# Performance work log

Hardware: AMD Instinct MI355X
Metric: run time of the kernel (lower is better)

Reference implementation:

```python
import jax, jax.numpy as jnp
import numpy as np

BN_EPS = 1e-6
SOFTMAX_EPS = 1e-8
D = 64      # fingerprint_dim
BD = 12     # bond_dim
N_ATOM = 10000
N_EDGE = 40000


def _bn(x, gamma, beta, mean, var):
    # BatchNorm1d in inference mode (running stats)
    return (x - mean) / jnp.sqrt(var + BN_EPS) * gamma + beta


def setup_inputs() -> dict:
    key = jax.random.key(0)
    ks = jax.random.split(key, 16)
    inp = {
        "atom": jax.random.normal(ks[0], (N_ATOM, D), dtype=jnp.float32),
        "bond_index": jax.random.randint(ks[1], (N_EDGE, 2), 0, N_ATOM, dtype=jnp.int64),
        "bond": jax.random.normal(ks[2], (N_EDGE, BD), dtype=jnp.float32),
        # encoder: Linear(bond_dim, D*D) + BatchNorm1d(D*D)
        "enc_W": jax.random.normal(ks[3], (D * D, BD), dtype=jnp.float32) * (1.0 / np.sqrt(BD)),
        "enc_b": jnp.zeros((D * D,), dtype=jnp.float32),
        "enc_gamma": jnp.ones((D * D,), dtype=jnp.float32),
        "enc_beta": jnp.zeros((D * D,), dtype=jnp.float32),
        "enc_mean": jnp.zeros((D * D,), dtype=jnp.float32),
        "enc_var": jnp.ones((D * D,), dtype=jnp.float32),
        # align: Linear(2*D, 1)
        "align_W": jax.random.normal(ks[4], (1, 2 * D), dtype=jnp.float32) * (1.0 / np.sqrt(2 * D)),
        "align_b": jnp.zeros((1,), dtype=jnp.float32),
        # attend: Linear(D, D) + BatchNorm1d(D), no activation
        "att_W": jax.random.normal(ks[5], (D, D), dtype=jnp.float32) * (1.0 / np.sqrt(D)),
        "att_b": jnp.zeros((D,), dtype=jnp.float32),
        "att_gamma": jnp.ones((D,), dtype=jnp.float32),
        "att_beta": jnp.zeros((D,), dtype=jnp.float32),
        "att_mean": jnp.zeros((D,), dtype=jnp.float32),
        "att_var": jnp.ones((D,), dtype=jnp.float32),
        # GRUCell(D, D)
        "gru_W_ih": jax.random.normal(ks[6], (3 * D, D), dtype=jnp.float32) * (1.0 / np.sqrt(D)),
        "gru_W_hh": jax.random.normal(ks[7], (3 * D, D), dtype=jnp.float32) * (1.0 / np.sqrt(D)),
        "gru_b_ih": jnp.zeros((3 * D,), dtype=jnp.float32),
        "gru_b_hh": jnp.zeros((3 * D,), dtype=jnp.float32),
    }
    return inp


def reference(atom, bond_index, bond,
              enc_W, enc_b, enc_gamma, enc_beta, enc_mean, enc_var,
              align_W, align_b,
              att_W, att_b, att_gamma, att_beta, att_mean, att_var,
              gru_W_ih, gru_W_hh, gru_b_ih, gru_b_hh):
    num_atom, d = atom.shape
    tgt = bond_index[:, 0]  # target atom of each edge
    nbr = bond_index[:, 1]  # neighbor atom of each edge

    # encoder: relu(BN(linear(bond))) -> per-edge [d, d] bond matrix
    enc = jax.nn.relu(_bn(bond @ enc_W.T + enc_b, enc_gamma, enc_beta, enc_mean, enc_var))
    enc = enc.reshape(-1, d, d)  # [E, d, d]

    # gather neighbor atoms, per-edge matvec through bond matrix
    neighbor = jnp.einsum('ed,edf->ef', atom[nbr], enc)  # [E, d]

    # attention logits (dropout is identity in eval)
    feat = jnp.concatenate([atom[tgt], neighbor], axis=-1)  # [E, 2d]
    score = jax.nn.leaky_relu(feat @ align_W.T + align_b, negative_slope=0.01)  # [E, 1]

    # segment softmax over target atoms
    mx = jax.ops.segment_max(score, tgt, num_segments=num_atom)  # [N, 1]
    ex = jnp.exp(score - mx[tgt])
    denom = jax.ops.segment_sum(ex, tgt, num_segments=num_atom)[tgt] + SOFTMAX_EPS
    attn = ex / denom  # [E, 1]

    # attend: BN(linear(neighbor)) (no activation), weighted scatter-add
    attd = _bn(neighbor @ att_W.T + att_b, att_gamma, att_beta, att_mean, att_var)
    context = jax.ops.segment_sum(attn * attd, tgt, num_segments=num_atom)  # [N, d]
    context = jax.nn.elu(context)

    # GRUCell(context, atom)
    gi = context @ gru_W_ih.T + gru_b_ih  # [N, 3d]
    gh = atom @ gru_W_hh.T + gru_b_hh     # [N, 3d]
    i_r, i_z, i_n = jnp.split(gi, 3, axis=-1)
    h_r, h_z, h_n = jnp.split(gh, 3, axis=-1)
    r = jax.nn.sigmoid(i_r + h_r)
    z = jax.nn.sigmoid(i_z + h_z)
    n = jnp.tanh(i_n + r * h_n)
    return (1.0 - z) * n + z * atom
```

## Files before the change

kernel.cpp:

```cpp
#include <hip/hip_runtime.h>
#include <math.h>

#define NA 10000
#define NE 40000

typedef float f4 __attribute__((ext_vector_type(4)));
typedef float f16v __attribute__((ext_vector_type(16)));
typedef int   i4 __attribute__((ext_vector_type(4)));
typedef __bf16 bf16x8 __attribute__((ext_vector_type(8)));

union U8 { unsigned short us[8]; bf16x8 v; };

static __device__ __forceinline__ unsigned short bf_rne(float x){
  unsigned u = __float_as_uint(x);
  unsigned r = (u + 0x7fffu + ((u>>16)&1u)) >> 16;
  return (unsigned short)r;
}
static __device__ __forceinline__ float bf_to_f(unsigned short h){
  return __uint_as_float(((unsigned)h)<<16);
}

__global__ __launch_bounds__(256) void k_pre(
  const float* __restrict__ encW, const float* __restrict__ encB,
  const float* __restrict__ eg, const float* __restrict__ ebt,
  const float* __restrict__ e_mn, const float* __restrict__ e_vr,
  const float* __restrict__ attW, const float* __restrict__ attB,
  const float* __restrict__ agm, const float* __restrict__ abt,
  const float* __restrict__ amn, const float* __restrict__ avr,
  const float* __restrict__ wih, const float* __restrict__ whh,
  const int* __restrict__ bidx, const float* __restrict__ atom,
  const float* __restrict__ alW,
  unsigned short* __restrict__ Bh, unsigned short* __restrict__ Bl,
  unsigned short* __restrict__ aBh, unsigned short* __restrict__ aBl,
  float* __restrict__ attBf, float* __restrict__ wT,
  float* __restrict__ p, int* __restrict__ cnt)
{
  int tid = threadIdx.x;
  int gid = blockIdx.x*256 + tid;
  int gstride = gridDim.x*256;
  for (int i=gid; i<65536; i+=gstride){
    int j = i&7, ll = (i>>3)&63, t = i>>9;
    int d = t>>1, ft = t&1;
    int k = ((ll>>5)<<3)+j;
    int n = d*64 + ft*32 + (ll&31);
    float s = eg[n]*rsqrtf(e_vr[n]+1e-6f);
    unsigned short vh=0, vl=0;
    if (k<12){
      float wv = encW[n*12+k]*s;
      unsigned short hi = bf_rne(wv);
      vh = hi; vl = bf_rne(wv - bf_to_f(hi));
    } else if (k==12){
      float b = (encB[n]-e_mn[n])*s + ebt[n];
      unsigned short hi = bf_rne(b);
      vh = hi; vl = bf_rne(b - bf_to_f(hi));
    }
    Bh[i] = vh; Bl[i] = vl;
  }
  for (int i=gid; i<4096; i+=gstride){
    int j=i&7, l=(i>>3)&63, t=i>>9;
    int kk=t>>1, nt=t&1;
    int k = kk*16 + ((l>>5)<<3) + j;
    int n = nt*32 + (l&31);
    float s = agm[n]*rsqrtf(avr[n]+1e-6f);
    float wv = attW[n*64+k]*s;
    unsigned short hi = bf_rne(wv);
    aBh[i]=hi; aBl[i]=bf_rne(wv - bf_to_f(hi));
  }
  for (int f=gid; f<64; f+=gstride){
    float s = agm[f]*rsqrtf(avr[f]+1e-6f);
    attBf[f] = (attB[f]-amn[f])*s + abt[f];
  }
  for (int i=gid; i<24576; i+=gstride){
    int j=i&3, f=(i>>2)&63, idx2=i>>8;
    int g=idx2>>4, kg=idx2&15, k=kg*4+j;
    wT[i] = (g<3)? wih[(g*64+f)*64+k] : whh[((g-3)*64+f)*64+k];
  }
  {
    int wid = gid>>6;
    int l = tid&63;
    float wl = alW[l];
    for (int a=wid; a<NA; a+=(gstride>>6)){
      float v = wl*atom[(size_t)a*64+l];
      v += __shfl_xor(v,1);  v += __shfl_xor(v,2);
      v += __shfl_xor(v,4);  v += __shfl_xor(v,8);
      v += __shfl_xor(v,16); v += __shfl_xor(v,32);
      if (l==0) p[a]=v;
    }
  }
  for (int e=gid; e<NE; e+=gstride) atomicAdd(&cnt[bidx[e*2]],1);
}

__global__ __launch_bounds__(256) void k_scan(const int* __restrict__ cnt,
                                              int* __restrict__ rowstart,
                                              int* __restrict__ wofs)
{
  __shared__ int sPart[256];
  int t = threadIdx.x;
  int base = t*40;
  i4 buf[10];
  int sum = 0;
  if (base < NA){
    const i4* cp = (const i4*)(cnt + base);
    #pragma unroll
    for (int i=0;i<10;i++) buf[i] = cp[i];
    #pragma unroll
    for (int i=0;i<10;i++) sum += buf[i].x+buf[i].y+buf[i].z+buf[i].w;
  }
  sPart[t]=sum;
  __syncthreads();
  for (int off=1; off<256; off<<=1){
    int v = (t>=off)? sPart[t-off] : 0;
    __syncthreads();
    sPart[t]+=v;
    __syncthreads();
  }
  int run = sPart[t]-sum;
  if (base < NA){
    #pragma unroll
    for (int i=0;i<10;i++){
      i4 b=buf[i], o;
      o.x=run; run+=b.x; o.y=run; run+=b.y;
      o.z=run; run+=b.z; o.w=run; run+=b.w;
      ((i4*)(rowstart+base))[i]=o;
      ((i4*)(wofs+base))[i]=o;
    }
  }
  if (t==0) rowstart[NA]=NE;
}

__global__ __launch_bounds__(256) void k_scatter(const int* __restrict__ bidx,
                                                 int* __restrict__ wofs,
                                                 int* __restrict__ elist)
{
  int e = blockIdx.x*256 + threadIdx.x;
  if (e < NE){
    int tg = bidx[e*2];
    int pos = atomicAdd(&wofs[tg],1);
    elist[pos]=e;
  }
}

__global__ __launch_bounds__(256) void k_edge(
  const float* __restrict__ atom, const int* __restrict__ bidx, const float* __restrict__ bond,
  const unsigned short* __restrict__ Bh, const unsigned short* __restrict__ Bl,
  const int* __restrict__ elist, float* __restrict__ nbC)
{
  __shared__ float sA[2304];
  __shared__ float sP[4096];
  __shared__ int   sEl[32];
  __shared__ int   sNbr[32];

  int tid = threadIdx.x;
  int l = tid & 63;
  int w = tid >> 6;
  int g = l >> 5;
  int em = l & 31;
  int E0 = blockIdx.x * 32;

  if (tid < 32){
    int e = elist[E0+tid];
    sEl[tid] = e;
    sNbr[tid] = bidx[e*2+1];
  }
  __syncthreads();
  for (int i=tid; i<2048; i+=256){
    int le=i>>6, d=i&63;
    sA[d*36+le] = atom[(size_t)sNbr[le]*64 + d];
  }

  U8 A1, A2;
  {
    const f4* bp = (const f4*)(bond + (size_t)sEl[em]*12);
    f4 b0=bp[0], b1v=bp[1], b2v=bp[2];
    float bv[12] = {b0.x,b0.y,b0.z,b0.w,b1v.x,b1v.y,b1v.z,b1v.w,b2v.x,b2v.y,b2v.z,b2v.w};
    unsigned short hi[12], lo2[12];
    #pragma unroll
    for (int j=0;j<12;j++){ hi[j]=bf_rne(bv[j]); lo2[j]=bf_rne(bv[j]-bf_to_f(hi[j])); }
    #pragma unroll
    for (int j=0;j<8;j++){
      int k = g*8+j;
      A1.us[j] = (k<12)? hi[k] : (k==12? (unsigned short)0x3F80 : (unsigned short)0);
      A2.us[j] = (k<12)? lo2[k] : (unsigned short)0;
    }
  }
  __syncthreads();

  int ft = w & 1;
  int dbase = (w >> 1) * 32;

  f4 nacc[4];
  #pragma unroll
  for (int q=0;q<4;q++) nacc[q] = (f4){0.f,0.f,0.f,0.f};
  f16v cz;
  #pragma unroll
  for (int r=0;r<16;r++) cz[r] = 0.f;

  U8 cbh, cbl;
  cbh.v = *(const bf16x8*)(Bh + ((size_t)((dbase*2+ft)*64 + l))*8);
  cbl.v = *(const bf16x8*)(Bl + ((size_t)((dbase*2+ft)*64 + l))*8);

  #pragma unroll 2
  for (int dd=0; dd<32; dd++){
    int d = dbase + dd;
    int dn = (dd<31)? d+1 : d;
    U8 nbh, nbl;
    nbh.v = *(const bf16x8*)(Bh + ((size_t)((dn*2+ft)*64 + l))*8);
    nbl.v = *(const bf16x8*)(Bl + ((size_t)((dn*2+ft)*64 + l))*8);

    f4 ldA[4];
    #pragma unroll
    for (int q=0;q<4;q++) ldA[q] = *(const f4*)&sA[d*36 + 8*q + 4*g];

    f16v c;
    c = __builtin_amdgcn_mfma_f32_32x32x16_bf16(A1.v, cbh.v, cz, 0,0,0);
    c = __builtin_amdgcn_mfma_f32_32x32x16_bf16(A2.v, cbh.v, c, 0,0,0);
    c = __builtin_amdgcn_mfma_f32_32x32x16_bf16(A1.v, cbl.v, c, 0,0,0);
    #pragma unroll
    for (int r=0;r<16;r++){
      float ev = fmaxf(c[r], 0.f);
      nacc[r>>2][r&3] = fmaf(ldA[r>>2][r&3], ev, nacc[r>>2][r&3]);
    }
    cbh = nbh; cbl = nbl;
  }

  #pragma unroll
  for (int r=0;r<16;r++)
    sP[w*1024 + r*64 + l] = nacc[r>>2][r&3];
  __syncthreads();

  if (w < 2){
    #pragma unroll 4
    for (int r=0;r<16;r++){
      int idx = r*64 + l;
      float v = sP[w*1024 + idx] + sP[(w+2)*1024 + idx];
      int m = (r&3) + ((r>>2)<<3) + ((l>>5)<<2);
      int f = (w<<5) + (l&31);
      nbC[(size_t)(E0+m)*64 + f] = v;
    }
  }
}

__global__ __launch_bounds__(256) void k_zq(
  const float* __restrict__ nbC,
  const unsigned short* __restrict__ aBh, const unsigned short* __restrict__ aBl,
  const float* __restrict__ alW,
  float* __restrict__ zC, float* __restrict__ qv)
{
  __shared__ float sNb[64*68];
  int tid = threadIdx.x;
  int l = tid & 63;
  int w = tid >> 6;
  int g = l >> 5;
  int em = l & 31;
  int E0 = blockIdx.x * 64;

  for (int i=tid; i<4096; i+=256){
    int le=i>>6, f=i&63;
    sNb[le*68+f] = nbC[(size_t)(E0+le)*64 + f];
  }
  __syncthreads();

  {
    float alwn = alW[64+l];
    #pragma unroll 4
    for (int i=0;i<16;i++){
      int le = w*16 + i;
      float qq = sNb[le*68 + l] * alwn;
      qq += __shfl_xor(qq,1);  qq += __shfl_xor(qq,2);
      qq += __shfl_xor(qq,4);  qq += __shfl_xor(qq,8);
      qq += __shfl_xor(qq,16); qq += __shfl_xor(qq,32);
      if (l==0) qv[E0+le] = qq;
    }
  }

  {
    f16v c;
    #pragma unroll
    for (int r=0;r<16;r++) c[r] = 0.f;
    int mt2 = w>>1, nt = w&1;
    #pragma unroll
    for (int kk=0; kk<4; kk++){
      const float* src = &sNb[(mt2*32+em)*68 + kk*16 + g*8];
      f4 x0 = *(const f4*)src;
      f4 x1 = *(const f4*)(src+4);
      U8 Ah, Al;
      #pragma unroll
      for (int j=0;j<4;j++){
        unsigned short h0 = bf_rne(x0[j]);
        Ah.us[j] = h0; Al.us[j] = bf_rne(x0[j]-bf_to_f(h0));
        unsigned short h1 = bf_rne(x1[j]);
        Ah.us[4+j] = h1; Al.us[4+j] = bf_rne(x1[j]-bf_to_f(h1));
      }
      U8 bh, bl;
      bh.v = *(const bf16x8*)(aBh + ((size_t)((kk*2+nt)*64 + l))*8);
      bl.v = *(const bf16x8*)(aBl + ((size_t)((kk*2+nt)*64 + l))*8);
      c = __builtin_amdgcn_mfma_f32_32x32x16_bf16(Ah.v, bh.v, c, 0,0,0);
      c = __builtin_amdgcn_mfma_f32_32x32x16_bf16(Al.v, bh.v, c, 0,0,0);
      c = __builtin_amdgcn_mfma_f32_32x32x16_bf16(Ah.v, bl.v, c, 0,0,0);
    }
    #pragma unroll
    for (int r=0;r<16;r++){
      int row = (r&3) + ((r>>2)<<3) + ((l>>5)<<2);
      zC[(size_t)(E0 + mt2*32 + row)*64 + nt*32 + (l&31)] = c[r];
    }
  }
}

__global__ __launch_bounds__(256, 4) void k_gru(
  const float* __restrict__ atom, const float* __restrict__ zC,
  const int* __restrict__ rowstart, const float* __restrict__ p,
  const float* __restrict__ qv, const float* __restrict__ alB,
  const float* __restrict__ attBf, const float* __restrict__ wT,
  const float* __restrict__ bih, const float* __restrict__ bhh,
  float* __restrict__ out)
{
  __shared__ float sc[4][2][64];
  __shared__ float shh[4][2][64];
  int tid = threadIdx.x;
  int l = tid & 63;
  int w = tid >> 6;
  int base = blockIdx.x*8 + w*2;
  float bias = attBf[l];
  float ab = alB[0];

  #pragma unroll
  for (int aa=0; aa<2; aa++){
    int a = base + aa;
    float cf=0.f, hf=0.f;
    if (a < NA){
      hf = atom[(size_t)a*64 + l];
      int d0 = rowstart[a];
      int deg = rowstart[a+1] - d0;
      if (deg > 0){
        float pa = p[a] + ab;
        float mx = -1e30f;
        #pragma unroll 1
        for (int i=0;i<deg;i++){
          float s = pa + qv[d0+i];
          s = (s>0.f)? s : 0.01f*s;
          mx = fmaxf(mx, s);
        }
        float dn = 0.f, y = 0.f;
        #pragma unroll 1
        for (int i=0;i<deg;i++){
          float s = pa + qv[d0+i];
          s = (s>0.f)? s : 0.01f*s;
          float ex = __expf(s - mx);
          dn += ex;
          y = fmaf(ex, zC[(size_t)(d0+i)*64 + l], y);
        }
        cf = (y + dn*bias)/(dn + 1e-8f);
        cf = (cf>0.f)? cf : expm1f(cf);
      }
    }
    sc[w][aa][l] = cf; shh[w][aa][l] = hf;
  }
  __syncthreads();

  float acc[6][2];
  #pragma unroll
  for (int gg=0;gg<6;gg++){ acc[gg][0]=0.f; acc[gg][1]=0.f; }

  #pragma unroll 2
  for (int kg=0; kg<16; kg++){
    f4 wv[6];
    #pragma unroll
    for (int gg=0;gg<6;gg++) wv[gg] = *(const f4*)&wT[(size_t)((gg*16+kg)*64 + l)*4];
    #pragma unroll
    for (int aa=0;aa<2;aa++){
      f4 cv = *(const f4*)&sc[w][aa][kg*4];
      f4 hv = *(const f4*)&shh[w][aa][kg*4];
      #pragma unroll
      for (int j=0;j<4;j++){
        acc[0][aa] = fmaf(cv[j], wv[0][j], acc[0][aa]);
        acc[1][aa] = fmaf(cv[j], wv[1][j], acc[1][aa]);
        acc[2][aa] = fmaf(cv[j], wv[2][j], acc[2][aa]);
        acc[3][aa] = fmaf(hv[j], wv[3][j], acc[3][aa]);
        acc[4][aa] = fmaf(hv[j], wv[4][j], acc[4][aa]);
        acc[5][aa] = fmaf(hv[j], wv[5][j], acc[5][aa]);
      }
    }
  }

  float b0 = bih[l], b1 = bih[64+l], b2 = bih[128+l];
  float h0 = bhh[l], h1 = bhh[64+l], h2 = bhh[128+l];
  #pragma unroll
  for (int aa=0;aa<2;aa++){
    int a = base + aa;
    if (a < NA){
      float hf = shh[w][aa][l];
      float r = 1.f/(1.f + expf(-(acc[0][aa] + b0 + acc[3][aa] + h0)));
      float z = 1.f/(1.f + expf(-(acc[1][aa] + b1 + acc[4][aa] + h1)));
      float n = tanhf(acc[2][aa] + b2 + r*(acc[5][aa] + h2));
      out[(size_t)a*64 + l] = (1.f - z)*n + z*hf;
    }
  }
}

extern "C" void kernel_launch(void* const* d_in, const int* in_sizes, int n_in,
                              void* d_out, int out_size, void* d_ws, size_t ws_size,
                              hipStream_t stream) {
  const float* atom = (const float*)d_in[0];
  const int*   bidx = (const int*)  d_in[1];
  const float* bond = (const float*)d_in[2];
  const float* encW = (const float*)d_in[3];
  const float* encB = (const float*)d_in[4];
  const float* eg   = (const float*)d_in[5];
  const float* ebt  = (const float*)d_in[6];
  const float* e_mn = (const float*)d_in[7];
  const float* e_vr = (const float*)d_in[8];
  const float* alW  = (const float*)d_in[9];
  const float* alB  = (const float*)d_in[10];
  const float* atW  = (const float*)d_in[11];
  const float* atB  = (const float*)d_in[12];
  const float* agm  = (const float*)d_in[13];
  const float* abt  = (const float*)d_in[14];
  const float* amn  = (const float*)d_in[15];
  const float* avr  = (const float*)d_in[16];
  const float* wih  = (const float*)d_in[17];
  const float* whh  = (const float*)d_in[18];
  const float* bih  = (const float*)d_in[19];
  const float* bhh  = (const float*)d_in[20];

  float* ws = (float*)d_ws;
  unsigned short* Bh  = (unsigned short*)(ws + 0);
  unsigned short* Bl  = (unsigned short*)(ws + 32768);
  unsigned short* aBh = (unsigned short*)(ws + 65536);
  unsigned short* aBl = (unsigned short*)(ws + 67584);
  float* attBf   = ws + 69632;
  float* wT      = ws + 69696;
  float* p       = ws + 94272;
  int*   cnt     = (int*)(ws + 104288);
  int*   rowstart= (int*)(ws + 114304);
  int*   wofs    = (int*)(ws + 124320);
  int*   elist   = (int*)(ws + 134336);
  float* qv      = ws + 174336;
  float* nbC     = ws + 214336;
  float* outp    = (float*)d_out;

  hipMemsetAsync(cnt, 0, NA*sizeof(int), stream);
  k_pre<<<512, 256, 0, stream>>>(encW,encB,eg,ebt,e_mn,e_vr,
                                 atW,atB,agm,abt,amn,avr,
                                 wih,whh,bidx,atom,alW,
                                 Bh,Bl,aBh,aBl,attBf,wT,p,cnt);
  k_scan<<<1, 256, 0, stream>>>(cnt, rowstart, wofs);
  k_scatter<<<(NE+255)/256, 256, 0, stream>>>(bidx, wofs, elist);
  k_edge<<<1250, 256, 0, stream>>>(atom, bidx, bond, Bh, Bl, elist, nbC);
  k_zq<<<625, 256, 0, stream>>>(nbC, aBh, aBl, alW, nbC , qv);
  k_gru<<<1250, 256, 0, stream>>>(atom, nbC, rowstart, p, qv, alB,
                                  attBf, wT, bih, bhh, outp);
}
```

Before: 186.6 us.

## Fuse degree histogram and prefix scan into block 0 of preprocessing kernel

Removes the global-memory atomic histogram, the memset and the separate single-block scan kernel. Block 0 of k_pre now builds the per-target histogram with LDS atomics over all 40000 edges and then scans it in shared memory to produce rowstart and wofs. This saves one kernel launch and one memset. The cost is that one block must serially process every edge, which could make it the critical path of k_pre. The scan also loses its vectorized loads.

Result: slower. 212.5 us (+13.9%).

```diff
diff --git a/kernel.cpp b/kernel.cpp
--- a/kernel.cpp
+++ b/kernel.cpp
@@ -33,8 +33,9 @@
   unsigned short* __restrict__ Bh, unsigned short* __restrict__ Bl,
   unsigned short* __restrict__ aBh, unsigned short* __restrict__ aBl,
   float* __restrict__ attBf, float* __restrict__ wT,
-  float* __restrict__ p, int* __restrict__ cnt)
+  float* __restrict__ p, int* __restrict__ rowstart, int* __restrict__ wofs)
 {
+  __shared__ int sH[10240 + 256];
   int tid = threadIdx.x;
   int gid = blockIdx.x*256 + tid;
   int gstride = gridDim.x*256;
@@ -87,45 +88,39 @@
       if (l==0) p[a]=v;
     }
   }
-  for (int e=gid; e<NE; e+=gstride) atomicAdd(&cnt[bidx[e*2]],1);
-}
-
-__global__ __launch_bounds__(256) void k_scan(const int* __restrict__ cnt,
-                                              int* __restrict__ rowstart,
-                                              int* __restrict__ wofs)
-{
-  __shared__ int sPart[256];
-  int t = threadIdx.x;
-  int base = t*40;
-  i4 buf[10];
-  int sum = 0;
-  if (base < NA){
-    const i4* cp = (const i4*)(cnt + base);
-    #pragma unroll
-    for (int i=0;i<10;i++) buf[i] = cp[i];
-    #pragma unroll
-    for (int i=0;i<10;i++) sum += buf[i].x+buf[i].y+buf[i].z+buf[i].w;
-  }
-  sPart[t]=sum;
-  __syncthreads();
-  for (int off=1; off<256; off<<=1){
-    int v = (t>=off)? sPart[t-off] : 0;
+  if (blockIdx.x == 0){
+    for (int i=tid; i<NA; i+=256) sH[i]=0;
     __syncthreads();
-    sPart[t]+=v;
+    for (int it=0; it<NE; it+=2048){
+      int e0 = it + tid*8;
+      #pragma unroll
+      for (int j=0;j<8;j++){
+        int e = e0 + j;
+        if (e < NE) atomicAdd(&sH[bidx[e*2]], 1);
+      }
+    }
     __syncthreads();
-  }
-  int run = sPart[t]-sum;
-  if (base < NA){
-    #pragma unroll
-    for (int i=0;i<10;i++){
-      i4 b=buf[i], o;
-      o.x=run; run+=b.x; o.y=run; run+=b.y;
-      o.z=run; run+=b.z; o.w=run; run+=b.w;
-      ((i4*)(rowstart+base))[i]=o;
-      ((i4*)(wofs+base))[i]=o;
-    }
-  }
-  if (t==0) rowstart[NA]=NE;
+    int* sPart = sH + 10240;
+    int base = tid*40;
+    int hi2 = base+40; if (hi2>NA) hi2=NA; int lo2 = (base>NA)? NA : base;
+    int sum = 0;
+    for (int i=lo2;i<hi2;i++) sum += sH[i];
+    sPart[tid]=sum;
+    __syncthreads();
+    for (int off=1; off<256; off<<=1){
+      int v = (tid>=off)? sPart[tid-off] : 0;
+      __syncthreads();
+      sPart[tid]+=v;
+      __syncthreads();
+    }
+    int run = sPart[tid]-sum;
+    for (int i=lo2;i<hi2;i++){
+      int c = sH[i];
+      rowstart[i]=run; wofs[i]=run;
+      run += c;
+    }
+    if (tid==0) rowstart[NA]=NE;
+  }
 }
 
 __global__ __launch_bounds__(256) void k_scatter(const int* __restrict__ bidx,
@@ -430,7 +425,6 @@
   float* attBf   = ws + 69632;
   float* wT      = ws + 69696;
   float* p       = ws + 94272;
-  int*   cnt     = (int*)(ws + 104288);
   int*   rowstart= (int*)(ws + 114304);
   int*   wofs    = (int*)(ws + 124320);
   int*   elist   = (int*)(ws + 134336);
@@ -438,12 +432,10 @@
   float* nbC     = ws + 214336;
   float* outp    = (float*)d_out;
 
-  hipMemsetAsync(cnt, 0, NA*sizeof(int), stream);
   k_pre<<<512, 256, 0, stream>>>(encW,encB,eg,ebt,e_mn,e_vr,
                                  atW,atB,agm,abt,amn,avr,
                                  wih,whh,bidx,atom,alW,
-                                 Bh,Bl,aBh,aBl,attBf,wT,p,cnt);
-  k_scan<<<1, 256, 0, stream>>>(cnt, rowstart, wofs);
+                                 Bh,Bl,aBh,aBl,attBf,wT,p,rowstart,wofs);
   k_scatter<<<(NE+255)/256, 256, 0, stream>>>(bidx, wofs, elist);
   k_edge<<<1250, 256, 0, stream>>>(atom, bidx, bond, Bh, Bl, elist, nbC);
   k_zq<<<625, 256, 0, stream>>>(nbC, aBh, aBl, alW, nbC , qv);
```
